# Kernel tuning notes

Hardware: AMD Instinct MI355X
Metric: run time of the kernel (lower is better)

## Reference

```python
import jax, jax.numpy as jnp
import numpy as np

NEG_SLOPE = 0.01  # nn.LeakyReLU default


def preprocess_adj(A):
    # D^-1/2 A D^-1/2, expressed as row/col broadcast scaling (same math as
    # the original diag_embed + two matmuls, without the O(N^3) waste)
    d = jnp.sum(A, axis=-1)
    d_inv_sqrt = d ** -0.5
    d_inv_sqrt = jnp.where(jnp.isinf(d_inv_sqrt), 0.0, d_inv_sqrt)
    return d_inv_sqrt[..., :, None] * A * d_inv_sqrt[..., None, :]


def gcn_layer(X, A_norm, W, b, residual=False):
    H = jax.nn.leaky_relu(jnp.einsum('bnd,df->bnf', X, W) + b, NEG_SLOPE)
    out = jnp.einsum('bnm,bmf->bnf', A_norm, H)
    if residual:
        out = out + X
    return out


def setup_inputs() -> dict:
    key = jax.random.key(0)
    ks = jax.random.split(key, 8)
    B, N, D_IN, D_H, D_OUT = 8, 2048, 128, 128, 128
    scale_in = 1.0 / np.sqrt(D_IN)
    scale_h = 1.0 / np.sqrt(D_H)
    return {
        'X': jax.random.normal(ks[0], (B, N, D_IN), dtype=jnp.float32),
        'adj': jax.random.uniform(ks[1], (B, N, N), dtype=jnp.float32),
        'W1': jax.random.uniform(ks[2], (D_IN, D_H), minval=-scale_in, maxval=scale_in),
        'b1': jax.random.uniform(ks[3], (D_H,), minval=-scale_in, maxval=scale_in),
        'W2': jax.random.uniform(ks[4], (D_H, D_H), minval=-scale_h, maxval=scale_h),
        'b2': jax.random.uniform(ks[5], (D_H,), minval=-scale_h, maxval=scale_h),
        'W3': jax.random.uniform(ks[6], (D_H, D_OUT), minval=-scale_h, maxval=scale_h),
        'b3': jax.random.uniform(ks[7], (D_OUT,), minval=-scale_h, maxval=scale_h),
    }


def reference(X, adj, W1, b1, W2, b2, W3, b3):
    # Original recomputes preprocess_adj in every layer; result is identical,
    # we honor the math (compute once since adj is unchanged across layers).
    A_norm = preprocess_adj(adj)
    X = gcn_layer(X, A_norm, W1, b1, residual=False)   # GCNLayer (norm defaults False)
    X = gcn_layer(X, A_norm, W2, b2, residual=True)    # Residual_GCNLayer
    X = gcn_layer(X, A_norm, W3, b3, residual=False)   # GCNLayer
    return X
```

## Files before the change

### kernel.cpp

```cpp
#include <hip/hip_runtime.h>


typedef short bf16x8 __attribute__((ext_vector_type(8)));
typedef float f32x4 __attribute__((ext_vector_type(4)));

static __device__ __forceinline__ float bf2f(unsigned short h) {
    union { unsigned int u; float f; } v; v.u = ((unsigned int)h) << 16; return v.f;
}
static __device__ __forceinline__ unsigned short f2bf(float x) {
    union { float f; unsigned int u; } v; v.f = x;
    return (unsigned short)((v.u + 0x7FFFu + ((v.u >> 16) & 1u)) >> 16);
}

static __device__ __forceinline__ void gl2lds16(const unsigned short* g,
                                                unsigned short* l) {
    __builtin_amdgcn_global_load_lds(
        (const __attribute__((address_space(1))) unsigned int*)g,
        (__attribute__((address_space(3))) unsigned int*)l, 16, 0, 0);
}

__global__ __launch_bounds__(256) void k_pre(const float* __restrict__ adj,
                                             const float* __restrict__ W1,
                                             const float* __restrict__ W2,
                                             const float* __restrict__ W3,
                                             const float* __restrict__ b1,
                                             const float* __restrict__ b2,
                                             const float* __restrict__ b3,
                                             float* __restrict__ dinv,
                                             unsigned short* __restrict__ adjb,
                                             unsigned short* __restrict__ WT,
                                             float* __restrict__ biasf) {
    if (blockIdx.x >= 16384) {
        const int e = (blockIdx.x - 16384) * 256 + threadIdx.x;
        if (e < 49152) {
            const int w = e >> 14, r = e & 16383;
            const int f = r & 127, k = r >> 7;
            const float* W = (w == 0) ? W1 : ((w == 1) ? W2 : W3);
            WT[w * 16384 + f * 128 + k] = f2bf(W[r]);
        } else if (e < 49536) {
            const int idx = e - 49152;
            const float* bp = (idx < 128) ? b1 : ((idx < 256) ? b2 : b3);
            biasf[idx] = bp[idx & 127];
        }
        return;
    }
    const int row = blockIdx.x;
    const size_t base = (size_t)row * 2048 + threadIdx.x * 8;
    const float4 a = *(const float4*)(adj + base);
    const float4 b = *(const float4*)(adj + base + 4);
    float s = a.x + a.y + a.z + a.w + b.x + b.y + b.z + b.w;
    union { uint4 u; unsigned short h[8]; } pk;
    pk.h[0] = f2bf(a.x); pk.h[1] = f2bf(a.y); pk.h[2] = f2bf(a.z); pk.h[3] = f2bf(a.w);
    pk.h[4] = f2bf(b.x); pk.h[5] = f2bf(b.y); pk.h[6] = f2bf(b.z); pk.h[7] = f2bf(b.w);
    *(uint4*)(adjb + base) = pk.u;
#pragma unroll
    for (int off = 32; off > 0; off >>= 1) s += __shfl_down(s, off);
    __shared__ float ws[4];
    if ((threadIdx.x & 63) == 0) ws[threadIdx.x >> 6] = s;
    __syncthreads();
    if (threadIdx.x == 0) {
        float t = ws[0] + ws[1] + ws[2] + ws[3];
        dinv[row] = (t > 0.f) ? rsqrtf(t) : 0.f;
    }
}

template <int AEXT>
__global__ __launch_bounds__(256) void k_gxw(const void* __restrict__ Asrc,
                                             const unsigned short* __restrict__ WTb,
                                             const float* __restrict__ biasf,
                                             const float* __restrict__ dinv,
                                             unsigned short* __restrict__ HsT) {
    constexpr int LDK = 136;
    __shared__ unsigned short Bs[128 * LDK];

    const int tid  = threadIdx.x;
    const int wave = tid >> 6;
    const int lane = tid & 63;
    const int n_   = lane & 15;
    const int q    = lane >> 4;
    const int wm   = wave >> 1;
    const int ch   = wave & 1;

    const int r0 = blockIdx.x * 32;

#pragma unroll
    for (int it = 0; it < 8; ++it) {
        int task = tid + it * 256;
        int f  = task >> 4;
        int cj = (task & 15) * 8;
        *(uint4*)(&Bs[f * LDK + cj]) = *(const uint4*)(WTb + f * 128 + cj);
    }
    __syncthreads();

    const int arow = r0 + wm * 16 + n_;
    bf16x8 av[4];
#pragma unroll
    for (int s = 0; s < 4; ++s) {
        if (AEXT) {
            const float* p = (const float*)Asrc + (size_t)arow * 128 + s * 32 + q * 8;
            float4 uu = ((const float4*)p)[0], w = ((const float4*)p)[1];
            union { bf16x8 v; unsigned short h[8]; } r;
            r.h[0] = f2bf(uu.x); r.h[1] = f2bf(uu.y); r.h[2] = f2bf(uu.z); r.h[3] = f2bf(uu.w);
            r.h[4] = f2bf(w.x);  r.h[5] = f2bf(w.y);  r.h[6] = f2bf(w.z);  r.h[7] = f2bf(w.w);
            av[s] = r.v;
        } else {
            av[s] = *(const bf16x8*)((const unsigned short*)Asrc + (size_t)arow * 128 + s * 32 + q * 8);
        }
    }

    f32x4 acc[4];
#pragma unroll
    for (int i = 0; i < 4; ++i) acc[i] = (f32x4){0.f, 0.f, 0.f, 0.f};
#pragma unroll
    for (int s = 0; s < 4; ++s) {
#pragma unroll
        for (int nt = 0; nt < 4; ++nt) {
            bf16x8 bv = *(const bf16x8*)(&Bs[(ch * 64 + nt * 16 + n_) * LDK + s * 32 + q * 8]);
            acc[nt] = __builtin_amdgcn_mfma_f32_16x16x32_bf16(av[s], bv, acc[nt], 0, 0, 0);
        }
    }

    const int rbase = r0 + wm * 16 + q * 4;
    float dsc[4];
#pragma unroll
    for (int r = 0; r < 4; ++r) dsc[r] = dinv[rbase + r];
    const int b  = rbase >> 11;
    const int jb = rbase & 2047;
    unsigned short* Hb = HsT + (size_t)b * (128 * 2048);
#pragma unroll
    for (int nt = 0; nt < 4; ++nt) {
        const int f = ch * 64 + nt * 16 + n_;
        const float bf = biasf[f];
        unsigned short pk[4];
#pragma unroll
        for (int r = 0; r < 4; ++r) {
            float v = acc[nt][r] + bf;
            v = (v > 0.f) ? v : 0.01f * v;
            pk[r] = f2bf(v * dsc[r]);
        }
        uint2 uo;
        uo.x = (unsigned int)pk[0] | ((unsigned int)pk[1] << 16);
        uo.y = (unsigned int)pk[2] | ((unsigned int)pk[3] << 16);
        *(uint2*)(Hb + (size_t)f * 2048 + jb) = uo;
    }
}

template <int MODE, int OUT32>
__global__ __launch_bounds__(512, 1) void k_gah(const unsigned short* __restrict__ adjb,
                                                const unsigned short* __restrict__ HsT,
                                                const float* __restrict__ dinv,
                                                const unsigned short* __restrict__ resid,
                                                void* __restrict__ outp) {
    constexpr int ABUFE = 64 * 64;
    constexpr int BBUFE = 128 * 64;
    constexpr int BUFE  = ABUFE + BBUFE;
    __shared__ unsigned short Sm[3 * BUFE];

    const int tid  = threadIdx.x;
    const int wave = tid >> 6;
    const int lane = tid & 63;
    const int n_   = lane & 15;
    const int q    = lane >> 4;
    const int wm   = wave >> 2;
    const int wn   = wave & 3;

    const int bb = blockIdx.x;
    const int b  = bb & 7;
    const int rt = bb >> 3;
    const int row0 = b * 2048 + rt * 64;

    const unsigned short* Ag = adjb + (size_t)row0 * 2048;
    const unsigned short* Bg = HsT + (size_t)b * (128 * 2048);

    const int lr  = lane >> 3;
    const int sch = (lane & 7) ^ lr;
    const unsigned short* Asg = Ag + (size_t)(wave * 8 + lr) * 2048 + sch * 8;
    const int dstA = wave * 512;
    const unsigned short* Bsg0 = Bg + (size_t)(wave * 16 + lr) * 2048 + sch * 8;
    const unsigned short* Bsg1 = Bsg0 + 8 * 2048;
    const int dstB = ABUFE + wave * 1024;

    const int swz = n_ & 7;
    int aoff[2][2], boff[2][2];
#pragma unroll
    for (int mi = 0; mi < 2; ++mi)
#pragma unroll
        for (int s = 0; s < 2; ++s)
            aoff[mi][s] = (wm * 32 + mi * 16 + n_) * 64 + (((s * 4 + q) ^ swz) * 8);
#pragma unroll
    for (int nj = 0; nj < 2; ++nj)
#pragma unroll
        for (int s = 0; s < 2; ++s)
            boff[nj][s] = ABUFE + (wn * 32 + nj * 16 + n_) * 64 + (((s * 4 + q) ^ swz) * 8);

    f32x4 acc[2][2];
#pragma unroll
    for (int i = 0; i < 2; ++i)
#pragma unroll
        for (int j = 0; j < 2; ++j) acc[i][j] = (f32x4){0.f, 0.f, 0.f, 0.f};

#pragma unroll
    for (int t = 0; t < 3; ++t) {
        const int kofs = t * 64;
        unsigned short* base = &Sm[t * BUFE];
        gl2lds16(Asg + kofs, base + dstA);
        gl2lds16(Bsg0 + kofs, base + dstB);
        gl2lds16(Bsg1 + kofs, base + dstB + 512);
    }

    int cur = 0;
#pragma unroll 1
    for (int t = 0; t < 32; ++t) {
        asm volatile("s_waitcnt vmcnt(6)" ::: "memory");
        __builtin_amdgcn_s_barrier();
        asm volatile("" ::: "memory");
        const unsigned short* sb = &Sm[cur * BUFE];
#pragma unroll
        for (int s = 0; s < 2; ++s) {
            bf16x8 a0 = *(const bf16x8*)(sb + aoff[0][s]);
            bf16x8 a1 = *(const bf16x8*)(sb + aoff[1][s]);
            bf16x8 b0 = *(const bf16x8*)(sb + boff[0][s]);
            bf16x8 b1 = *(const bf16x8*)(sb + boff[1][s]);
            acc[0][0] = __builtin_amdgcn_mfma_f32_16x16x32_bf16(a0, b0, acc[0][0], 0, 0, 0);
            acc[1][0] = __builtin_amdgcn_mfma_f32_16x16x32_bf16(a1, b0, acc[1][0], 0, 0, 0);
            acc[0][1] = __builtin_amdgcn_mfma_f32_16x16x32_bf16(a0, b1, acc[0][1], 0, 0, 0);
            acc[1][1] = __builtin_amdgcn_mfma_f32_16x16x32_bf16(a1, b1, acc[1][1], 0, 0, 0);
        }
        asm volatile("" ::: "memory");
        __builtin_amdgcn_s_barrier();
        asm volatile("" ::: "memory");
        {
            const int kofs = ((t + 3) & 31) * 64;
            unsigned short* base = &Sm[cur * BUFE];
            gl2lds16(Asg + kofs, base + dstA);
            gl2lds16(Bsg0 + kofs, base + dstB);
            gl2lds16(Bsg1 + kofs, base + dstB + 512);
        }
        cur = (cur == 2) ? 0 : cur + 1;
    }

    const int rb = row0 + wm * 32 + q * 4;
    float dsc[2][4];
#pragma unroll
    for (int mi = 0; mi < 2; ++mi)
#pragma unroll
        for (int r = 0; r < 4; ++r) dsc[mi][r] = dinv[rb + mi * 16 + r];
#pragma unroll
    for (int mi = 0; mi < 2; ++mi) {
#pragma unroll
        for (int nj = 0; nj < 2; ++nj) {
            const int f = wn * 32 + nj * 16 + n_;
#pragma unroll
            for (int r = 0; r < 4; ++r) {
                const size_t gr = (size_t)(rb + mi * 16 + r);
                float v = acc[mi][nj][r] * dsc[mi][r];
                if (MODE == 2) v += bf2f(resid[gr * 128 + f]);
                if (OUT32) ((float*)outp)[gr * 128 + f] = v;
                else ((unsigned short*)outp)[gr * 128 + f] = f2bf(v);
            }
        }
    }
}

extern "C" void kernel_launch(void* const* d_in, const int* in_sizes, int n_in,
                              void* d_out, int out_size, void* d_ws, size_t ws_size,
                              hipStream_t stream) {
    const float* X   = (const float*)d_in[0];
    const float* adj = (const float*)d_in[1];
    const float* W1  = (const float*)d_in[2];
    const float* b1  = (const float*)d_in[3];
    const float* W2  = (const float*)d_in[4];
    const float* b2  = (const float*)d_in[5];
    const float* W3  = (const float*)d_in[6];
    const float* b3  = (const float*)d_in[7];

    char* ws = (char*)d_ws;
    unsigned short* adjb  = (unsigned short*)ws;
    float*          dinv  = (float*)(ws + (64u << 20));
    float*          biasf = (float*)(ws + (64u << 20) + (64u << 10));
    unsigned short* WT    = (unsigned short*)(ws + (64u << 20) + (128u << 10));
    unsigned short* HsT   = (unsigned short*)(ws + (64u << 20) + (256u << 10));
    unsigned short* Xa    = (unsigned short*)(ws + (68u << 20) + (256u << 10));
    unsigned short* X2    = (unsigned short*)(ws + (72u << 20) + (256u << 10));

    k_pre<<<16578, 256, 0, stream>>>(adj, W1, W2, W3, b1, b2, b3, dinv, adjb, WT, biasf);

    k_gxw<1><<<512, 256, 0, stream>>>(X, WT, biasf, dinv, HsT);
    k_gah<1, 0><<<256, 512, 0, stream>>>(adjb, HsT, dinv, nullptr, Xa);
    k_gxw<0><<<512, 256, 0, stream>>>(Xa, WT + 16384, biasf + 128, dinv, HsT);
    k_gah<2, 0><<<256, 512, 0, stream>>>(adjb, HsT, dinv, Xa, X2);
    k_gxw<0><<<512, 256, 0, stream>>>(X2, WT + 32768, biasf + 256, dinv, HsT);
    k_gah<1, 1><<<256, 512, 0, stream>>>(adjb, HsT, dinv, nullptr, (float*)d_out);
}
```

Baseline: 271.1 us.

## Use four-stage LDS ring and interleave async loads with MFMA

The shared-memory ring in the aggregation kernel grows from three stages to four, so the next tile's global-to-LDS loads can go into a free slot and be issued in the middle of the MFMA sequence instead of after the trailing barrier. MFMA groups are wrapped in s_setprio to favour matrix work while loads are in flight. This targets the serialisation between compute and load issue in the K loop, at the cost of more LDS per block. The loop still ends with a barrier, and the vmcnt(6) wait count is left unchanged.

```diff
diff --git a/kernel.cpp b/kernel.cpp
--- a/kernel.cpp
+++ b/kernel.cpp
@@ -154,7 +154,7 @@
     constexpr int ABUFE = 64 * 64;
     constexpr int BBUFE = 128 * 64;
     constexpr int BUFE  = ABUFE + BBUFE;
-    __shared__ unsigned short Sm[3 * BUFE];
+    __shared__ unsigned short Sm[4 * BUFE];
 
     const int tid  = threadIdx.x;
     const int wave = tid >> 6;
@@ -208,35 +208,43 @@
         gl2lds16(Bsg1 + kofs, base + dstB + 512);
     }
 
-    int cur = 0;
 #pragma unroll 1
     for (int t = 0; t < 32; ++t) {
         asm volatile("s_waitcnt vmcnt(6)" ::: "memory");
         __builtin_amdgcn_s_barrier();
         asm volatile("" ::: "memory");
-        const unsigned short* sb = &Sm[cur * BUFE];
-#pragma unroll
-        for (int s = 0; s < 2; ++s) {
-            bf16x8 a0 = *(const bf16x8*)(sb + aoff[0][s]);
-            bf16x8 a1 = *(const bf16x8*)(sb + aoff[1][s]);
-            bf16x8 b0 = *(const bf16x8*)(sb + boff[0][s]);
-            bf16x8 b1 = *(const bf16x8*)(sb + boff[1][s]);
+        const unsigned short* sb = &Sm[(t & 3) * BUFE];
+        unsigned short* sw = &Sm[((t + 3) & 3) * BUFE];
+        const int kofs = ((t + 3) & 31) * 64;
+        {
+            bf16x8 a0 = *(const bf16x8*)(sb + aoff[0][0]);
+            bf16x8 a1 = *(const bf16x8*)(sb + aoff[1][0]);
+            bf16x8 b0 = *(const bf16x8*)(sb + boff[0][0]);
+            bf16x8 b1 = *(const bf16x8*)(sb + boff[1][0]);
+            gl2lds16(Asg + kofs, sw + dstA);
+            __builtin_amdgcn_s_setprio(1);
             acc[0][0] = __builtin_amdgcn_mfma_f32_16x16x32_bf16(a0, b0, acc[0][0], 0, 0, 0);
             acc[1][0] = __builtin_amdgcn_mfma_f32_16x16x32_bf16(a1, b0, acc[1][0], 0, 0, 0);
             acc[0][1] = __builtin_amdgcn_mfma_f32_16x16x32_bf16(a0, b1, acc[0][1], 0, 0, 0);
             acc[1][1] = __builtin_amdgcn_mfma_f32_16x16x32_bf16(a1, b1, acc[1][1], 0, 0, 0);
+            __builtin_amdgcn_s_setprio(0);
+        }
+        {
+            bf16x8 a0 = *(const bf16x8*)(sb + aoff[0][1]);
+            bf16x8 a1 = *(const bf16x8*)(sb + aoff[1][1]);
+            bf16x8 b0 = *(const bf16x8*)(sb + boff[0][1]);
+            bf16x8 b1 = *(const bf16x8*)(sb + boff[1][1]);
+            gl2lds16(Bsg0 + kofs, sw + dstB);
+            gl2lds16(Bsg1 + kofs, sw + dstB + 512);
+            __builtin_amdgcn_s_setprio(1);
+            acc[0][0] = __builtin_amdgcn_mfma_f32_16x16x32_bf16(a0, b0, acc[0][0], 0, 0, 0);
+            acc[1][0] = __builtin_amdgcn_mfma_f32_16x16x32_bf16(a1, b0, acc[1][0], 0, 0, 0);
+            acc[0][1] = __builtin_amdgcn_mfma_f32_16x16x32_bf16(a0, b1, acc[0][1], 0, 0, 0);
+            acc[1][1] = __builtin_amdgcn_mfma_f32_16x16x32_bf16(a1, b1, acc[1][1], 0, 0, 0);
+            __builtin_amdgcn_s_setprio(0);
         }
         asm volatile("" ::: "memory");
         __builtin_amdgcn_s_barrier();
-        asm volatile("" ::: "memory");
-        {
-            const int kofs = ((t + 3) & 31) * 64;
-            unsigned short* base = &Sm[cur * BUFE];
-            gl2lds16(Asg + kofs, base + dstA);
-            gl2lds16(Bsg0 + kofs, base + dstB);
-            gl2lds16(Bsg1 + kofs, base + dstB + 512);
-        }
-        cur = (cur == 2) ? 0 : cur + 1;
     }
 
     const int rb = row0 + wm * 32 + q * 4;
```

Measured after the change: 273.1 us. No clear change (+0.7%).

## Fuse next layer's X·W transform into the aggregation kernel epilogue

Applied to the files above, without the earlier changes.

Adds a k_gahx kernel that, after computing the A·H aggregation for a 64-row tile, stages the bf16 result and the next layer's transposed weights in shared memory. It then performs the next layer's X·W + bias + LeakyReLU + D^-1/2 scaling with MFMA in the same kernel, writing the transposed H for the next layer directly. This removes two k_gxw launches and the round trip of the intermediate X through global memory, except where it is still needed as the residual. It uses ping-pong HsT buffers and adds epilogue work and LDS pressure to the aggregation kernel.

```diff
diff --git a/kernel.cpp b/kernel.cpp
--- a/kernel.cpp
+++ b/kernel.cpp
@@ -145,6 +145,7 @@
     }
 }
 
+
 template <int MODE, int OUT32>
 __global__ __launch_bounds__(512, 1) void k_gah(const unsigned short* __restrict__ adjb,
                                                 const unsigned short* __restrict__ HsT,
@@ -258,6 +259,188 @@
                 if (OUT32) ((float*)outp)[gr * 128 + f] = v;
                 else ((unsigned short*)outp)[gr * 128 + f] = f2bf(v);
             }
+        }
+    }
+}
+
+template <int MODE, int WRX>
+__global__ __launch_bounds__(512, 1) void k_gahx(const unsigned short* __restrict__ adjb,
+                                                 const unsigned short* __restrict__ HsTin,
+                                                 const float* __restrict__ dinv,
+                                                 const unsigned short* __restrict__ resid,
+                                                 unsigned short* __restrict__ Xout,
+                                                 const unsigned short* __restrict__ WTn,
+                                                 const float* __restrict__ biasn,
+                                                 unsigned short* __restrict__ HsTout) {
+    constexpr int ABUFE = 64 * 64;
+    constexpr int BBUFE = 128 * 64;
+    constexpr int BUFE  = ABUFE + BBUFE;
+    constexpr int LDX   = 136;
+    constexpr int XW0   = 10240;
+    __shared__ unsigned short Sm[3 * BUFE];
+
+    const int tid  = threadIdx.x;
+    const int wave = tid >> 6;
+    const int lane = tid & 63;
+    const int n_   = lane & 15;
+    const int q    = lane >> 4;
+    const int wm   = wave >> 2;
+    const int wn   = wave & 3;
+
+    const int bb = blockIdx.x;
+    const int b  = bb & 7;
+    const int rt = bb >> 3;
+    const int row0 = b * 2048 + rt * 64;
+
+    const unsigned short* Ag = adjb + (size_t)row0 * 2048;
+    const unsigned short* Bg = HsTin + (size_t)b * (128 * 2048);
+
+    const int lr  = lane >> 3;
+    const int sch = (lane & 7) ^ lr;
+    const unsigned short* Asg = Ag + (size_t)(wave * 8 + lr) * 2048 + sch * 8;
+    const int dstA = wave * 512;
+    const unsigned short* Bsg0 = Bg + (size_t)(wave * 16 + lr) * 2048 + sch * 8;
+    const unsigned short* Bsg1 = Bsg0 + 8 * 2048;
+    const int dstB = ABUFE + wave * 1024;
+
+    const int swz = n_ & 7;
+    int aoff[2][2], boff[2][2];
+#pragma unroll
+    for (int mi = 0; mi < 2; ++mi)
+#pragma unroll
+        for (int s = 0; s < 2; ++s)
+            aoff[mi][s] = (wm * 32 + mi * 16 + n_) * 64 + (((s * 4 + q) ^ swz) * 8);
+#pragma unroll
+    for (int nj = 0; nj < 2; ++nj)
+#pragma unroll
+        for (int s = 0; s < 2; ++s)
+            boff[nj][s] = ABUFE + (wn * 32 + nj * 16 + n_) * 64 + (((s * 4 + q) ^ swz) * 8);
+
+    f32x4 acc[2][2];
+#pragma unroll
+    for (int i = 0; i < 2; ++i)
+#pragma unroll
+        for (int j = 0; j < 2; ++j) acc[i][j] = (f32x4){0.f, 0.f, 0.f, 0.f};
+
+#pragma unroll
+    for (int t = 0; t < 3; ++t) {
+        const int kofs = t * 64;
+        unsigned short* base = &Sm[t * BUFE];
+        gl2lds16(Asg + kofs, base + dstA);
+        gl2lds16(Bsg0 + kofs, base + dstB);
+        gl2lds16(Bsg1 + kofs, base + dstB + 512);
+    }
+
+    int cur = 0;
+#pragma unroll 1
+    for (int t = 0; t < 32; ++t) {
+        asm volatile("s_waitcnt vmcnt(6)" ::: "memory");
+        __builtin_amdgcn_s_barrier();
+        asm volatile("" ::: "memory");
+        const unsigned short* sb = &Sm[cur * BUFE];
+#pragma unroll
+        for (int s = 0; s < 2; ++s) {
+            bf16x8 a0 = *(const bf16x8*)(sb + aoff[0][s]);
+            bf16x8 a1 = *(const bf16x8*)(sb + aoff[1][s]);
+            bf16x8 b0 = *(const bf16x8*)(sb + boff[0][s]);
+            bf16x8 b1 = *(const bf16x8*)(sb + boff[1][s]);
+            acc[0][0] = __builtin_amdgcn_mfma_f32_16x16x32_bf16(a0, b0, acc[0][0], 0, 0, 0);
+            acc[1][0] = __builtin_amdgcn_mfma_f32_16x16x32_bf16(a1, b0, acc[1][0], 0, 0, 0);
+            acc[0][1] = __builtin_amdgcn_mfma_f32_16x16x32_bf16(a0, b1, acc[0][1], 0, 0, 0);
+            acc[1][1] = __builtin_amdgcn_mfma_f32_16x16x32_bf16(a1, b1, acc[1][1], 0, 0, 0);
+        }
+        asm volatile("" ::: "memory");
+        __builtin_amdgcn_s_barrier();
+        asm volatile("" ::: "memory");
+        {
+            const int kofs = ((t + 3) & 31) * 64;
+            unsigned short* base = &Sm[cur * BUFE];
+            gl2lds16(Asg + kofs, base + dstA);
+            gl2lds16(Bsg0 + kofs, base + dstB);
+            gl2lds16(Bsg1 + kofs, base + dstB + 512);
+        }
+        cur = (cur == 2) ? 0 : cur + 1;
+    }
+
+    asm volatile("s_waitcnt vmcnt(0)" ::: "memory");
+    __syncthreads();
+
+    const int rb = row0 + wm * 32 + q * 4;
+    float dsc[2][4];
+#pragma unroll
+    for (int mi = 0; mi < 2; ++mi)
+#pragma unroll
+        for (int r = 0; r < 4; ++r) dsc[mi][r] = dinv[rb + mi * 16 + r];
+#pragma unroll
+    for (int mi = 0; mi < 2; ++mi) {
+#pragma unroll
+        for (int nj = 0; nj < 2; ++nj) {
+            const int f = wn * 32 + nj * 16 + n_;
+#pragma unroll
+            for (int r = 0; r < 4; ++r) {
+                const size_t gr = (size_t)(rb + mi * 16 + r);
+                float v = acc[mi][nj][r] * dsc[mi][r];
+                if (MODE == 2) v += bf2f(resid[gr * 128 + f]);
+                const unsigned short hv = f2bf(v);
+                if (WRX) Xout[gr * 128 + f] = hv;
+                Sm[(wm * 32 + mi * 16 + q * 4 + r) * LDX + f] = hv;
+            }
+        }
+    }
+    {
+        const int row = tid >> 2;
+        const int c0  = (tid & 3) * 32;
+        const unsigned short* src = WTn + row * 128 + c0;
+        unsigned short* dst = &Sm[XW0 + row * LDX + c0];
+#pragma unroll
+        for (int k = 0; k < 4; ++k)
+            *(uint4*)(dst + k * 8) = *(const uint4*)(src + k * 8);
+    }
+    __syncthreads();
+
+    const int jh = wave >> 2;
+    const int fq = wave & 3;
+    f32x4 ah[2][2];
+#pragma unroll
+    for (int i = 0; i < 2; ++i)
+#pragma unroll
+        for (int j = 0; j < 2; ++j) ah[i][j] = (f32x4){0.f, 0.f, 0.f, 0.f};
+#pragma unroll
+    for (int s = 0; s < 4; ++s) {
+        bf16x8 xa0 = *(const bf16x8*)(&Sm[(jh * 32 + n_) * LDX + s * 32 + q * 8]);
+        bf16x8 xa1 = *(const bf16x8*)(&Sm[(jh * 32 + 16 + n_) * LDX + s * 32 + q * 8]);
+        bf16x8 wb0 = *(const bf16x8*)(&Sm[XW0 + (fq * 32 + n_) * LDX + s * 32 + q * 8]);
+        bf16x8 wb1 = *(const bf16x8*)(&Sm[XW0 + (fq * 32 + 16 + n_) * LDX + s * 32 + q * 8]);
+        ah[0][0] = __builtin_amdgcn_mfma_f32_16x16x32_bf16(xa0, wb0, ah[0][0], 0, 0, 0);
+        ah[1][0] = __builtin_amdgcn_mfma_f32_16x16x32_bf16(xa1, wb0, ah[1][0], 0, 0, 0);
+        ah[0][1] = __builtin_amdgcn_mfma_f32_16x16x32_bf16(xa0, wb1, ah[0][1], 0, 0, 0);
+        ah[1][1] = __builtin_amdgcn_mfma_f32_16x16x32_bf16(xa1, wb1, ah[1][1], 0, 0, 0);
+    }
+    const int jg0 = row0 + jh * 32 + q * 4;
+    const int jb  = (row0 & 2047) + jh * 32 + q * 4;
+    float dh[2][4];
+#pragma unroll
+    for (int mi = 0; mi < 2; ++mi)
+#pragma unroll
+        for (int r = 0; r < 4; ++r) dh[mi][r] = dinv[jg0 + mi * 16 + r];
+    unsigned short* Hb = HsTout + (size_t)b * (128 * 2048);
+#pragma unroll
+    for (int mi = 0; mi < 2; ++mi) {
+#pragma unroll
+        for (int nj = 0; nj < 2; ++nj) {
+            const int f = fq * 32 + nj * 16 + n_;
+            const float bf = biasn[f];
+            unsigned short pk[4];
+#pragma unroll
+            for (int r = 0; r < 4; ++r) {
+                float v = ah[mi][nj][r] + bf;
+                v = (v > 0.f) ? v : 0.01f * v;
+                pk[r] = f2bf(v * dh[mi][r]);
+            }
+            uint2 uo;
+            uo.x = (unsigned int)pk[0] | ((unsigned int)pk[1] << 16);
+            uo.y = (unsigned int)pk[2] | ((unsigned int)pk[3] << 16);
+            *(uint2*)(Hb + (size_t)f * 2048 + jb + mi * 16) = uo;
         }
     }
 }
@@ -279,16 +462,16 @@
     float*          dinv  = (float*)(ws + (64u << 20));
     float*          biasf = (float*)(ws + (64u << 20) + (64u << 10));
     unsigned short* WT    = (unsigned short*)(ws + (64u << 20) + (128u << 10));
-    unsigned short* HsT   = (unsigned short*)(ws + (64u << 20) + (256u << 10));
-    unsigned short* Xa    = (unsigned short*)(ws + (68u << 20) + (256u << 10));
-    unsigned short* X2    = (unsigned short*)(ws + (72u << 20) + (256u << 10));
+    unsigned short* HsTa  = (unsigned short*)(ws + (64u << 20) + (256u << 10));
+    unsigned short* HsTb  = (unsigned short*)(ws + (68u << 20) + (256u << 10));
+    unsigned short* Xa    = (unsigned short*)(ws + (72u << 20) + (256u << 10));
 
     k_pre<<<16578, 256, 0, stream>>>(adj, W1, W2, W3, b1, b2, b3, dinv, adjb, WT, biasf);
 
-    k_gxw<1><<<512, 256, 0, stream>>>(X, WT, biasf, dinv, HsT);
-    k_gah<1, 0><<<256, 512, 0, stream>>>(adjb, HsT, dinv, nullptr, Xa);
-    k_gxw<0><<<512, 256, 0, stream>>>(Xa, WT + 16384, biasf + 128, dinv, HsT);
-    k_gah<2, 0><<<256, 512, 0, stream>>>(adjb, HsT, dinv, Xa, X2);
-    k_gxw<0><<<512, 256, 0, stream>>>(X2, WT + 32768, biasf + 256, dinv, HsT);
-    k_gah<1, 1><<<256, 512, 0, stream>>>(adjb, HsT, dinv, nullptr, (float*)d_out);
-}
+    k_gxw<1><<<512, 256, 0, stream>>>(X, WT, biasf, dinv, HsTa);
+    k_gahx<1, 1><<<256, 512, 0, stream>>>(adjb, HsTa, dinv, nullptr, Xa,
+                                          WT + 16384, biasf + 128, HsTb);
+    k_gahx<2, 0><<<256, 512, 0, stream>>>(adjb, HsTb, dinv, Xa, nullptr,
+                                          WT + 32768, biasf + 256, HsTa);
+    k_gah<1, 1><<<256, 512, 0, stream>>>(adjb, HsTa, dinv, nullptr, (float*)d_out);
+}
```

Result: faster. 262.1 us (-3.3%).
